# Kernel optimization log

Hardware: AMD Instinct MI355X
Metric: run time of the kernel (lower is better)

## Reference

```python
import jax, jax.numpy as jnp
import numpy as np
from jax import lax

NUM_GROUP = 512    # G: number of FPS centers
GROUP_SIZE = 32    # M: KNN neighbors per center


def setup_inputs() -> dict:
    key = jax.random.key(0)
    xyz = jax.random.normal(key, (32, 8192, 3), dtype=jnp.float32)  # B N 3
    return {"xyz": xyz}


def _fps(xyz, num_group):
    """Iterative farthest point sampling. xyz: [B,N,3] -> idx [B,G] int32.
    Deterministic start at point 0 (matching pointnet2-style fps)."""
    B, N, _ = xyz.shape

    def step(carry, _):
        dists, last_idx = carry                       # dists: [B,N] running min sq-dist
        last = xyz[jnp.arange(B), last_idx]           # [B,3] most recent center
        d = jnp.sum((xyz - last[:, None, :]) ** 2, axis=-1)  # [B,N]
        dists = jnp.minimum(dists, d)
        nxt = jnp.argmax(dists, axis=-1).astype(jnp.int32)   # farthest point
        return (dists, nxt), nxt

    init_idx = jnp.zeros((B,), jnp.int32)
    init_d = jnp.full((B, N), jnp.inf, xyz.dtype)
    (_, _), idxs = lax.scan(step, (init_d, init_idx), None, length=num_group - 1)
    return jnp.concatenate([init_idx[None, :], idxs], axis=0).T  # [B,G]


def reference(xyz):
    B, N, _ = xyz.shape
    G, M = NUM_GROUP, GROUP_SIZE

    fps_idx = _fps(xyz, G)                              # [B,G] int32
    center = xyz[jnp.arange(B)[:, None], fps_idx]       # [B,G,3]

    # KNN: for each center, k nearest points in xyz (squared euclidean)
    # dist2[b,g,n] = |c|^2 + |x|^2 - 2 c.x   -> [B,G,N]
    x2 = jnp.sum(xyz * xyz, axis=-1)                    # [B,N]
    c2 = jnp.sum(center * center, axis=-1)              # [B,G]
    dist2 = c2[:, :, None] + x2[:, None, :] - 2.0 * jnp.einsum('bgd,bnd->bgn', center, xyz)
    _, idx = lax.top_k(-dist2, M)                       # [B,G,M] nearest-first

    neighborhood = xyz[jnp.arange(B)[:, None, None], idx]   # [B,G,M,3]
    neighborhood = neighborhood - center[:, :, None, :]
    return neighborhood, center, fps_idx
```

## Files before the change

### kernel.cpp

```cpp
#include <hip/hip_runtime.h>
#include <math.h>

#define BATCH  32
#define NPTS   8192
#define NGROUP 512
#define MSIZE  32

#define FPS_THREADS 512
#define SXYZ_FLOATS (NPTS * 3)
#define DYN_LDS_BYTES (SXYZ_FLOATS * 4)

typedef float v2f __attribute__((ext_vector_type(2)));

template<int CTRL>
__device__ __forceinline__ float dpp_max_f32(float x) {
    int o = __builtin_amdgcn_update_dpp(0, __float_as_int(x), CTRL, 0xF, 0xF, true);
    float f = __int_as_float(o);
    return x > f ? x : f;
}
template<int CTRL>
__device__ __forceinline__ unsigned dpp_min_u32(unsigned x) {
    unsigned o = (unsigned)__builtin_amdgcn_update_dpp(0, (int)x, CTRL, 0xF, 0xF, true);
    return o < x ? o : x;
}
template<int CTRL>
__device__ __forceinline__ unsigned long long dpp_max_u64(unsigned long long k) {
    int lo2 = __builtin_amdgcn_update_dpp(0, (int)(unsigned)k,        CTRL, 0xF, 0xF, true);
    int hi2 = __builtin_amdgcn_update_dpp(0, (int)(unsigned)(k >> 32), CTRL, 0xF, 0xF, true);
    unsigned long long k2 = (((unsigned long long)(unsigned)hi2) << 32) | (unsigned)lo2;
    return k2 > k ? k2 : k;
}
template<int CTRL>
__device__ __forceinline__ unsigned dpp_min_u32_full(unsigned x) {
    unsigned o = (unsigned)__builtin_amdgcn_update_dpp(0, (int)x, CTRL, 0xF, 0xF, true);
    return o < x ? o : x;
}

__global__ __launch_bounds__(FPS_THREADS, 2)
void fps_kernel(const float* __restrict__ xyz,
                float* __restrict__ out_center,
                float* __restrict__ out_fps)
{
#pragma clang fp contract(off)
    extern __shared__ float sxyz[];
    __shared__ unsigned long long partial[2][8];

    const int b    = blockIdx.x;
    const int t    = threadIdx.x;
    const int lane = t & 63;
    const int wid  = t >> 6;
    const float* bp = xyz + (size_t)b * NPTS * 3;
    const float4* bp4 = reinterpret_cast<const float4*>(bp);
    float4* s4 = reinterpret_cast<float4*>(sxyz);

    v2f px2[8], py2[8], pz2[8], dist2[8];
    unsigned idxv[16];
    #pragma unroll
    for (int c = 0; c < 4; ++c) {
        int f4 = c * 1536 + t * 3;
        float4 A = bp4[f4 + 0];
        float4 B = bp4[f4 + 1];
        float4 C = bp4[f4 + 2];
        s4[f4 + 0] = A; s4[f4 + 1] = B; s4[f4 + 2] = C;
        int j0 = c * 2, j1 = c * 2 + 1;
        px2[j0] = (v2f){A.x, A.w};  py2[j0] = (v2f){A.y, B.x};  pz2[j0] = (v2f){A.z, B.y};
        px2[j1] = (v2f){B.z, C.y};  py2[j1] = (v2f){B.w, C.z};  pz2[j1] = (v2f){C.x, C.w};
        dist2[j0] = (v2f){INFINITY, INFINITY};
        dist2[j1] = (v2f){INFINITY, INFINITY};
        #pragma unroll
        for (int k = 0; k < 4; ++k)
            idxv[c*4 + k] = (unsigned)(c * 2048 + t * 4 + k);
    }
    __syncthreads();

    if (t == 0) {
        out_fps[(size_t)b * NGROUP] = 0.0f;
        out_center[(size_t)(b * NGROUP) * 3 + 0] = sxyz[0];
        out_center[(size_t)(b * NGROUP) * 3 + 1] = sxyz[1];
        out_center[(size_t)(b * NGROUP) * 3 + 2] = sxyz[2];
    }

    int last = 0;
    for (int g = 1; g < NGROUP; ++g) {
        const int p = g & 1;
        float lx = sxyz[last*3 + 0];
        float ly = sxyz[last*3 + 1];
        float lz = sxyz[last*3 + 2];

        #pragma unroll
        for (int j = 0; j < 8; ++j) {
            v2f dx = px2[j] - lx;
            v2f dy = py2[j] - ly;
            v2f dz = pz2[j] - lz;
            v2f t1 = dx * dx;
            v2f t2 = dy * dy;
            v2f t3 = dz * dz;
            v2f s  = t1 + t2;
            v2f d  = s + t3;
            dist2[j] = __builtin_elementwise_min(dist2[j], d);
        }
        v2f mm = dist2[0];
        #pragma unroll
        for (int j = 1; j < 8; ++j) mm = __builtin_elementwise_max(mm, dist2[j]);
        float m = fmaxf(mm.x, mm.y);
        m = dpp_max_f32<0xB1>(m);
        m = dpp_max_f32<0x4E>(m);
        m = dpp_max_f32<0x141>(m);
        m = dpp_max_f32<0x140>(m);
        m = dpp_max_f32<0x142>(m);
        m = dpp_max_f32<0x143>(m);
        float wmax = __int_as_float(__builtin_amdgcn_readlane(__float_as_int(m), 63));

        unsigned c0[16];
        #pragma unroll
        for (int j = 0; j < 8; ++j) {
            c0[2*j+0] = (dist2[j].x == wmax) ? idxv[2*j+0] : 0xFFFFFFFFu;
            c0[2*j+1] = (dist2[j].y == wmax) ? idxv[2*j+1] : 0xFFFFFFFFu;
        }
        #pragma unroll
        for (int s = 8; s >= 1; s >>= 1)
            #pragma unroll
            for (int i = 0; i < s; ++i)
                c0[i] = c0[i] < c0[i+s] ? c0[i] : c0[i+s];
        unsigned mi = c0[0];
        mi = dpp_min_u32<0xB1>(mi);
        mi = dpp_min_u32<0x4E>(mi);
        mi = dpp_min_u32<0x141>(mi);
        mi = dpp_min_u32<0x140>(mi);
        mi = dpp_min_u32<0x142>(mi);
        mi = dpp_min_u32<0x143>(mi);
        if (lane == 63) {
            unsigned long long key =
                (((unsigned long long)__float_as_uint(wmax)) << 32) | (unsigned)~mi;
            partial[p][wid] = key;
        }
        __syncthreads();

        unsigned long long kq = partial[p][lane & 7];
        kq = dpp_max_u64<0xB1>(kq);
        kq = dpp_max_u64<0x4E>(kq);
        kq = dpp_max_u64<0x141>(kq);
        int fi = (int)(~(unsigned)kq);
        last = fi;
        if (t == 0) {
            out_fps[(size_t)b * NGROUP + g] = (float)fi;
            out_center[((size_t)(b * NGROUP + g)) * 3 + 0] = sxyz[fi*3 + 0];
            out_center[((size_t)(b * NGROUP + g)) * 3 + 1] = sxyz[fi*3 + 1];
            out_center[((size_t)(b * NGROUP + g)) * 3 + 2] = sxyz[fi*3 + 2];
        }
    }
}

__global__ __launch_bounds__(256)
void knn_kernel(const float* __restrict__ xyz,
                const float* __restrict__ center,
                float* __restrict__ out_nbhd)
{
    const int lane = threadIdx.x & 63;
    const int gid  = blockIdx.x * 4 + (threadIdx.x >> 6);
    const int b    = gid >> 9;
    const float* bp = xyz + (size_t)b * NPTS * 3;
    const float4* bp4 = reinterpret_cast<const float4*>(bp);

    const float cx = center[(size_t)gid*3+0];
    const float cy = center[(size_t)gid*3+1];
    const float cz = center[(size_t)gid*3+2];

    unsigned kl[4];
    #pragma unroll
    for (int k = 0; k < 4; ++k) kl[k] = 0xFFFFFFFFu;

    for (int c = 0; c < 32; ++c) {
        int f4 = c * 192 + lane * 3;
        float4 a  = bp4[f4+0];
        float4 bq = bp4[f4+1];
        float4 cq = bp4[f4+2];
        unsigned p0 = (unsigned)(c * 256 + lane * 4);
        v2f xA = (v2f){a.x,  a.w},  yA = (v2f){a.y,  bq.x}, zA = (v2f){a.z,  bq.y};
        v2f xB = (v2f){bq.z, cq.y}, yB = (v2f){bq.w, cq.z}, zB = (v2f){cq.x, cq.w};
        v2f dxA = xA - cx, dyA = yA - cy, dzA = zA - cz;
        v2f dxB = xB - cx, dyB = yB - cy, dzB = zB - cz;
        v2f dA = dxA*dxA + dyA*dyA + dzA*dzA;
        v2f dB = dxB*dxB + dyB*dyB + dzB*dzB;
        float ds[4] = {dA.x, dA.y, dB.x, dB.y};
        #pragma unroll
        for (int k = 0; k < 4; ++k) {
            unsigned key = (__float_as_uint(ds[k]) & 0xFFFFE000u) | (p0 + k);
            if (key < kl[3]) {
                kl[3] = key;
                #pragma unroll
                for (int q = 3; q > 0; --q) {
                    if (kl[q] < kl[q-1]) {
                        unsigned tk = kl[q]; kl[q] = kl[q-1]; kl[q-1] = tk;
                    }
                }
            }
        }
    }

    int keep = 0;
    #pragma unroll 1
    for (int r = 0; r < MSIZE; ++r) {
        unsigned k = kl[0];
        k = dpp_min_u32_full<0xB1>(k);
        k = dpp_min_u32_full<0x4E>(k);
        k = dpp_min_u32_full<0x141>(k);
        k = dpp_min_u32_full<0x140>(k);
        {
            unsigned o = __shfl_xor(k, 16);
            k = o < k ? o : k;
            o = __shfl_xor(k, 32);
            k = o < k ? o : k;
        }
        if (lane == r) keep = (int)(k & 0x1FFFu);
        if (kl[0] == k) {
            kl[0] = kl[1]; kl[1] = kl[2]; kl[2] = kl[3];
            kl[3] = 0xFFFFFFFFu;
        }
    }

    if (lane < MSIZE) {
        size_t o = ((size_t)gid * MSIZE + lane) * 3;
        float x = bp[keep*3+0], y = bp[keep*3+1], z = bp[keep*3+2];
        out_nbhd[o+0] = x - cx;
        out_nbhd[o+1] = y - cy;
        out_nbhd[o+2] = z - cz;
    }
}

extern "C" void kernel_launch(void* const* d_in, const int* in_sizes, int n_in,
                              void* d_out, int out_size, void* d_ws, size_t ws_size,
                              hipStream_t stream)
{
    const float* xyz = (const float*)d_in[0];
    float* out        = (float*)d_out;
    float* out_nbhd   = out;
    float* out_center = out + (size_t)BATCH*NGROUP*MSIZE*3;
    float* out_fps    = out_center + (size_t)BATCH*NGROUP*3;

    hipFuncSetAttribute(reinterpret_cast<const void*>(fps_kernel),
                        hipFuncAttributeMaxDynamicSharedMemorySize,
                        DYN_LDS_BYTES);

    fps_kernel<<<dim3(BATCH), dim3(FPS_THREADS), DYN_LDS_BYTES, stream>>>(xyz, out_center, out_fps);
    knn_kernel<<<dim3(BATCH*NGROUP/4), dim3(256), 0, stream>>>(xyz, out_center, out_nbhd);
}
```

Measured before the change: 619.2 us.

## Use contiguous point ownership, ballot-based argmax and LDS atomicMax reduction in FPS

Each thread now owns 16 contiguous points, so the local index comes from the thread id plus a slot number and the per-thread index array goes away. The per-wave argmin-of-index DPP chain is replaced by a ballot that picks the first lane holding the maximum, followed by a readlane. The cross-wave reduction becomes an LDS atomicMax into a triple-buffered key, which removes the second DPP reduction over 64-bit keys. The aim is fewer instructions per FPS iteration. The risk is that 8 serialized LDS atomics per step cost more than the DPP work they replace.

```diff
diff --git a/kernel.cpp b/kernel.cpp
--- a/kernel.cpp
+++ b/kernel.cpp
@@ -17,18 +17,6 @@
     int o = __builtin_amdgcn_update_dpp(0, __float_as_int(x), CTRL, 0xF, 0xF, true);
     float f = __int_as_float(o);
     return x > f ? x : f;
-}
-template<int CTRL>
-__device__ __forceinline__ unsigned dpp_min_u32(unsigned x) {
-    unsigned o = (unsigned)__builtin_amdgcn_update_dpp(0, (int)x, CTRL, 0xF, 0xF, true);
-    return o < x ? o : x;
-}
-template<int CTRL>
-__device__ __forceinline__ unsigned long long dpp_max_u64(unsigned long long k) {
-    int lo2 = __builtin_amdgcn_update_dpp(0, (int)(unsigned)k,        CTRL, 0xF, 0xF, true);
-    int hi2 = __builtin_amdgcn_update_dpp(0, (int)(unsigned)(k >> 32), CTRL, 0xF, 0xF, true);
-    unsigned long long k2 = (((unsigned long long)(unsigned)hi2) << 32) | (unsigned)lo2;
-    return k2 > k ? k2 : k;
 }
 template<int CTRL>
 __device__ __forceinline__ unsigned dpp_min_u32_full(unsigned x) {
@@ -43,34 +31,33 @@
 {
 #pragma clang fp contract(off)
     extern __shared__ float sxyz[];
-    __shared__ unsigned long long partial[2][8];
+    __shared__ unsigned long long gkey[3];
 
     const int b    = blockIdx.x;
     const int t    = threadIdx.x;
     const int lane = t & 63;
-    const int wid  = t >> 6;
     const float* bp = xyz + (size_t)b * NPTS * 3;
     const float4* bp4 = reinterpret_cast<const float4*>(bp);
     float4* s4 = reinterpret_cast<float4*>(sxyz);
 
     v2f px2[8], py2[8], pz2[8], dist2[8];
-    unsigned idxv[16];
-    #pragma unroll
-    for (int c = 0; c < 4; ++c) {
-        int f4 = c * 1536 + t * 3;
-        float4 A = bp4[f4 + 0];
-        float4 B = bp4[f4 + 1];
-        float4 C = bp4[f4 + 2];
-        s4[f4 + 0] = A; s4[f4 + 1] = B; s4[f4 + 2] = C;
-        int j0 = c * 2, j1 = c * 2 + 1;
-        px2[j0] = (v2f){A.x, A.w};  py2[j0] = (v2f){A.y, B.x};  pz2[j0] = (v2f){A.z, B.y};
-        px2[j1] = (v2f){B.z, C.y};  py2[j1] = (v2f){B.w, C.z};  pz2[j1] = (v2f){C.x, C.w};
-        dist2[j0] = (v2f){INFINITY, INFINITY};
-        dist2[j1] = (v2f){INFINITY, INFINITY};
-        #pragma unroll
-        for (int k = 0; k < 4; ++k)
-            idxv[c*4 + k] = (unsigned)(c * 2048 + t * 4 + k);
-    }
+    {
+        float f[48];
+        #pragma unroll
+        for (int q = 0; q < 12; ++q) {
+            float4 v = bp4[t * 12 + q];
+            s4[t * 12 + q] = v;
+            f[q*4+0] = v.x; f[q*4+1] = v.y; f[q*4+2] = v.z; f[q*4+3] = v.w;
+        }
+        #pragma unroll
+        for (int j = 0; j < 8; ++j) {
+            px2[j] = (v2f){f[6*j+0], f[6*j+3]};
+            py2[j] = (v2f){f[6*j+1], f[6*j+4]};
+            pz2[j] = (v2f){f[6*j+2], f[6*j+5]};
+            dist2[j] = (v2f){INFINITY, INFINITY};
+        }
+    }
+    if (t == 0) { gkey[0] = 0; gkey[1] = 0; gkey[2] = 0; }
     __syncthreads();
 
     if (t == 0) {
@@ -82,7 +69,8 @@
 
     int last = 0;
     for (int g = 1; g < NGROUP; ++g) {
-        const int p = g & 1;
+        const int slot = g % 3;
+        const int nxt  = (g + 1) % 3;
         float lx = sxyz[last*3 + 0];
         float ly = sxyz[last*3 + 1];
         float lz = sxyz[last*3 + 2];
@@ -99,10 +87,16 @@
             v2f d  = s + t3;
             dist2[j] = __builtin_elementwise_min(dist2[j], d);
         }
-        v2f mm = dist2[0];
-        #pragma unroll
-        for (int j = 1; j < 8; ++j) mm = __builtin_elementwise_max(mm, dist2[j]);
-        float m = fmaxf(mm.x, mm.y);
+        v2f mm0 = __builtin_elementwise_max(dist2[0], dist2[1]);
+        v2f mm1 = __builtin_elementwise_max(dist2[2], dist2[3]);
+        v2f mm2 = __builtin_elementwise_max(dist2[4], dist2[5]);
+        v2f mm3 = __builtin_elementwise_max(dist2[6], dist2[7]);
+        v2f mma = __builtin_elementwise_max(mm0, mm1);
+        v2f mmb = __builtin_elementwise_max(mm2, mm3);
+        v2f mmc = __builtin_elementwise_max(mma, mmb);
+        float m_t = fmaxf(mmc.x, mmc.y);
+
+        float m = m_t;
         m = dpp_max_f32<0xB1>(m);
         m = dpp_max_f32<0x4E>(m);
         m = dpp_max_f32<0x141>(m);
@@ -111,35 +105,27 @@
         m = dpp_max_f32<0x143>(m);
         float wmax = __int_as_float(__builtin_amdgcn_readlane(__float_as_int(m), 63));
 
-        unsigned c0[16];
-        #pragma unroll
-        for (int j = 0; j < 8; ++j) {
-            c0[2*j+0] = (dist2[j].x == wmax) ? idxv[2*j+0] : 0xFFFFFFFFu;
-            c0[2*j+1] = (dist2[j].y == wmax) ? idxv[2*j+1] : 0xFFFFFFFFu;
-        }
-        #pragma unroll
-        for (int s = 8; s >= 1; s >>= 1)
-            #pragma unroll
-            for (int i = 0; i < s; ++i)
-                c0[i] = c0[i] < c0[i+s] ? c0[i] : c0[i+s];
-        unsigned mi = c0[0];
-        mi = dpp_min_u32<0xB1>(mi);
-        mi = dpp_min_u32<0x4E>(mi);
-        mi = dpp_min_u32<0x141>(mi);
-        mi = dpp_min_u32<0x140>(mi);
-        mi = dpp_min_u32<0x142>(mi);
-        mi = dpp_min_u32<0x143>(mi);
+        unsigned long long mask = __ballot(m_t == wmax);
+        int l = __ffsll((long long)mask) - 1;
+
+        unsigned lj = 0;
+        #pragma unroll
+        for (int j = 15; j >= 0; --j) {
+            float dj = (j & 1) ? dist2[j >> 1].y : dist2[j >> 1].x;
+            lj = (dj == wmax) ? (unsigned)j : lj;
+        }
+        unsigned idx = ((unsigned)t << 4) | lj;
+        unsigned widx = (unsigned)__builtin_amdgcn_readlane((int)idx, l);
+
         if (lane == 63) {
             unsigned long long key =
-                (((unsigned long long)__float_as_uint(wmax)) << 32) | (unsigned)~mi;
-            partial[p][wid] = key;
+                (((unsigned long long)__float_as_uint(wmax)) << 32) | (unsigned)~widx;
+            atomicMax(&gkey[slot], key);
+            if (t == 63) gkey[nxt] = 0;
         }
         __syncthreads();
 
-        unsigned long long kq = partial[p][lane & 7];
-        kq = dpp_max_u64<0xB1>(kq);
-        kq = dpp_max_u64<0x4E>(kq);
-        kq = dpp_max_u64<0x141>(kq);
+        unsigned long long kq = gkey[slot];
         int fi = (int)(~(unsigned)kq);
         last = fi;
         if (t == 0) {
```

Measured after the change: 576.7 us. -6.9%, faster.
